# Kernel optimization log

Measured on AMD Instinct MI355X. Metric: run time of the kernel, lower is better.

## Reference

```python
import jax, jax.numpy as jnp
import numpy as np

TOP_K = 2
E = 8      # num_experts
D = 1024   # model dim
F = 2048   # expert hidden dim = int(2*3072/3), already a multiple of 256
B, S = 2, 1024


def setup_inputs() -> dict:
    key = jax.random.key(0)
    ks = jax.random.split(key, 8)
    sc = 0.02
    return {
        "x_bsD": jax.random.normal(ks[0], (B, S, D), dtype=jnp.float32),
        "router_DE": jax.random.normal(ks[1], (D, E), dtype=jnp.float32) * sc,
        "w_in_shared_FD": jax.random.normal(ks[2], (F, D), dtype=jnp.float32) * sc,
        "w_out_shared_DF": jax.random.normal(ks[3], (D, F), dtype=jnp.float32) * sc,
        "w_swiglu_FD": jax.random.normal(ks[4], (F, D), dtype=jnp.float32) * sc,
        "w_in_eDF": jax.random.normal(ks[5], (E, D, F), dtype=jnp.float32) * sc,
        "w_swiglu_eDF": jax.random.normal(ks[6], (E, D, F), dtype=jnp.float32) * sc,
        "w_out_eFD": jax.random.normal(ks[7], (E, F, D), dtype=jnp.float32) * sc,
    }


def reference(x_bsD, router_DE, w_in_shared_FD, w_out_shared_DF, w_swiglu_FD,
              w_in_eDF, w_swiglu_eDF, w_out_eFD):
    b, s, d = x_bsD.shape
    x_aD = x_bsD.reshape(-1, d)                      # [a, D]
    a = x_aD.shape[0]

    # Router (token choice): top-k per token, others masked to -inf
    scores_aE = x_aD @ router_DE                      # [a, E]
    topv_aK, topi_aK = jax.lax.top_k(scores_aE, TOP_K)
    masked_aE = jnp.full_like(scores_aE, -jnp.inf)
    masked_aE = masked_aE.at[jnp.arange(a)[:, None], topi_aK].set(topv_aK)
    # sigmoid(-inf) == 0 -> non-selected (expert, token) pairs contribute nothing
    gates_Ea = jax.nn.sigmoid(masked_aE.astype(jnp.float32)).astype(x_aD.dtype).T  # [E, a]

    # Dispatch: router_indices_EG == arange(a) per expert, so gather == broadcast
    routed_in_EaD = x_aD[None, :, :] * gates_Ea[:, :, None]   # [E, a, D]
    routed_in_EaD = jax.lax.stop_gradient(routed_in_EaD)      # matches .detach()

    # Per-expert bmm SwiGLU
    mid_EaF = jnp.einsum('ead,edf->eaf', routed_in_EaD, w_in_eDF)
    sw_EaF = jnp.einsum('ead,edf->eaf', routed_in_EaD, w_swiglu_eDF)
    h_EaF = jax.nn.silu(mid_EaF) * sw_EaF
    out_EaD = jnp.einsum('eaf,efd->ead', h_EaF, w_out_eFD)

    # Shared expert (computed under torch.no_grad in the original)
    shared_aF = jax.nn.silu(x_aD @ w_in_shared_FD.T) * (x_aD @ w_swiglu_FD.T)
    shared_out_aD = jax.lax.stop_gradient(shared_aF @ w_out_shared_DF.T)

    # Combine: scatter_add with per-expert arange indices == sum over experts
    out_aD = shared_out_aD + jnp.sum(out_EaD, axis=0)
    return out_aD.reshape(b, s, d)
```

## Files before the change

kernel.cpp:

```cpp
#include <hip/hip_runtime.h>
#include <hip/hip_bf16.h>

#define A_TOK 2048
#define DDIM 1024
#define FDIM 2048
#define NEXP 8
#define NE9 9
#define SLOTS_R (2 * A_TOK)
#define SLOTS_T (SLOTS_R + A_TOK)
#define NB1 (2 * FDIM)

#define PREP_TRA_END 8192
#define PREP_TRB_END (PREP_TRA_END + 4096)
#define PREP_SH12_END (PREP_TRB_END + 1024)
#define PREP_SHOUT_END (PREP_SH12_END + 512)
#define PREP_NWG (PREP_SHOUT_END + 512)

typedef __attribute__((ext_vector_type(8))) short short8v;
typedef __attribute__((ext_vector_type(4))) float f32x4;
typedef __attribute__((ext_vector_type(4))) ushort ushort4v;

#define BARRIER() asm volatile("s_barrier" ::: "memory")
#define VMCNT(n) asm volatile("s_waitcnt vmcnt(" #n ")" ::: "memory")

__device__ __forceinline__ void lds16(const void* g, void* l) {
  __builtin_amdgcn_global_load_lds((const __attribute__((address_space(1))) void*)g,
                                   (__attribute__((address_space(3))) void*)l, 16, 0, 0);
}

__device__ __forceinline__ float sigmoidf_(float x) { return 1.f / (1.f + __expf(-x)); }
__device__ __forceinline__ ushort f2bf(float x) {
  __hip_bfloat16 b = __float2bfloat16(x);
  ushort u; __builtin_memcpy(&u, &b, 2); return u;
}
__device__ __forceinline__ float bf2f(ushort u) {
  union { unsigned int i; float f; } x; x.i = (unsigned int)u << 16; return x.f;
}

__global__ void k_prep(const float* __restrict__ w_in_e, const float* __restrict__ w_sw_e,
                       const float* __restrict__ w_out_e, const float* __restrict__ w_in_sh,
                       const float* __restrict__ w_sw_sh, const float* __restrict__ w_out_sh,
                       ushort* __restrict__ wt12, ushort* __restrict__ wt_out_t,
                       const float* __restrict__ x, const float* __restrict__ rw,
                       __hip_bfloat16* __restrict__ xbf, int* __restrict__ top_e,
                       float* __restrict__ top_g) {
  __shared__ ushort tile[64][68];
  int b = blockIdx.x, tid = threadIdx.x;
  if (b < PREP_TRA_END) {
    int z = b >> 9, t2 = b & 511;
    int e = z & 7, which = z >> 3;
    const float* in = (which ? w_sw_e : w_in_e) + (size_t)e * DDIM * FDIM;
    ushort* outb = wt12 + (size_t)e * NB1 * DDIM;
    int c0 = (t2 & 31) * 64, r0 = (t2 >> 5) * 64;
    int rr = tid >> 4, cq = tid & 15;
#pragma unroll
    for (int i = 0; i < 4; i++) {
      int r = i * 16 + rr;
      float4 v = *(const float4*)(in + (size_t)(r0 + r) * FDIM + c0 + cq * 4);
      ushort4v o = {f2bf(v.x), f2bf(v.y), f2bf(v.z), f2bf(v.w)};
      *(ushort4v*)&tile[r][cq * 4] = o;
    }
    __syncthreads();
    int cc = tid >> 4, rq = tid & 15;
#pragma unroll
    for (int i = 0; i < 4; i++) {
      int c = i * 16 + cc;
      int f = c0 + c;
      int rp = ((f >> 5) << 6) + (which << 5) + (f & 31);
      ushort4v o = {tile[rq * 4 + 0][c], tile[rq * 4 + 1][c],
                    tile[rq * 4 + 2][c], tile[rq * 4 + 3][c]};
      *(ushort4v*)(outb + (size_t)rp * DDIM + r0 + rq * 4) = o;
    }
  } else if (b < PREP_TRB_END) {
    int b2 = b - PREP_TRA_END;
    int z = b2 >> 9, t2 = b2 & 511;
    const float* in = w_out_e + (size_t)z * FDIM * DDIM;
    ushort* out = wt_out_t + (size_t)z * DDIM * FDIM;
    int c0 = (t2 & 15) * 64, r0 = (t2 >> 4) * 64;
    int rr = tid >> 4, cq = tid & 15;
#pragma unroll
    for (int i = 0; i < 4; i++) {
      int r = i * 16 + rr;
      float4 v = *(const float4*)(in + (size_t)(r0 + r) * DDIM + c0 + cq * 4);
      ushort4v o = {f2bf(v.x), f2bf(v.y), f2bf(v.z), f2bf(v.w)};
      *(ushort4v*)&tile[r][cq * 4] = o;
    }
    __syncthreads();
    int cc = tid >> 4, rq = tid & 15;
#pragma unroll
    for (int i = 0; i < 4; i++) {
      int c = i * 16 + cc;
      ushort4v o = {tile[rq * 4 + 0][c], tile[rq * 4 + 1][c],
                    tile[rq * 4 + 2][c], tile[rq * 4 + 3][c]};
      *(ushort4v*)(out + (size_t)(c0 + c) * FDIM + r0 + rq * 4) = o;
    }
  } else if (b < PREP_SH12_END) {
    int j = b - PREP_TRB_END;
    int rj = j * 4 + (tid >> 6);
    int l = tid & 63;
    int which = rj & 1, f = rj >> 1;
    const float* src = (which ? w_sw_sh : w_in_sh) + (size_t)f * DDIM;
    int rp = ((f >> 5) << 6) + (which << 5) + (f & 31);
    ushort* dst = wt12 + (size_t)NEXP * NB1 * DDIM + (size_t)rp * DDIM;
#pragma unroll
    for (int i = 0; i < 4; i++) {
      int q = l + 64 * i;
      float4 v = ((const float4*)src)[q];
      ushort4v o = {f2bf(v.x), f2bf(v.y), f2bf(v.z), f2bf(v.w)};
      ((ushort4v*)dst)[q] = o;
    }
  } else if (b < PREP_SHOUT_END) {
    int j = b - PREP_SH12_END;
    int d = j * 2 + (tid >> 7);
    int l = tid & 127;
    const float* src = w_out_sh + (size_t)d * FDIM;
    ushort* dst = wt_out_t + (size_t)NEXP * DDIM * FDIM + (size_t)d * FDIM;
#pragma unroll
    for (int i = 0; i < 4; i++) {
      int q = l + 128 * i;
      float4 v = ((const float4*)src)[q];
      ushort4v o = {f2bf(v.x), f2bf(v.y), f2bf(v.z), f2bf(v.w)};
      ((ushort4v*)dst)[q] = o;
    }
  } else {
    int j = b - PREP_SHOUT_END;
    int t = j * 4 + (tid >> 6);
    int l = tid & 63;
    const float* xr = x + (size_t)t * DDIM;
    float acc[NEXP];
#pragma unroll
    for (int e = 0; e < NEXP; e++) acc[e] = 0.f;
#pragma unroll
    for (int i = 0; i < 16; i++) {
      int d = i * 64 + l;
      float v = xr[d];
      xbf[(size_t)t * DDIM + d] = __float2bfloat16(v);
      const float* rr = rw + (size_t)d * NEXP;
#pragma unroll
      for (int e = 0; e < NEXP; e++) acc[e] += v * rr[e];
    }
#pragma unroll
    for (int e = 0; e < NEXP; e++) {
#pragma unroll
      for (int s = 32; s > 0; s >>= 1) acc[e] += __shfl_xor(acc[e], s);
    }
    if (l == 0) {
      float b1 = -1e30f, b2 = -1e30f;
      int i1 = 0, i2 = 0;
#pragma unroll
      for (int e = 0; e < NEXP; e++) {
        float v = acc[e];
        if (v > b1) { b2 = b1; i2 = i1; b1 = v; i1 = e; }
        else if (v > b2) { b2 = v; i2 = e; }
      }
      top_e[t * 2 + 0] = i1; top_e[t * 2 + 1] = i2;
      top_g[t * 2 + 0] = sigmoidf_(b1); top_g[t * 2 + 1] = sigmoidf_(b2);
    }
  }
}

__global__ void k_scan(const int* __restrict__ top_e, int* __restrict__ counts,
                       int* __restrict__ offs, int* __restrict__ cursor) {
  __shared__ int hist[NEXP];
  int tid = threadIdx.x;
  if (tid < NEXP) hist[tid] = 0;
  __syncthreads();
  for (int i = tid; i < A_TOK * 2; i += 256) atomicAdd(&hist[top_e[i]], 1);
  __syncthreads();
  if (tid == 0) {
    int s = 0;
    for (int e = 0; e < NEXP; e++) { counts[e] = hist[e]; offs[e] = s; s += hist[e]; cursor[e] = 0; }
    counts[NEXP] = A_TOK;
    offs[NEXP] = s;
  }
}

__global__ void k_dispatch(const float* __restrict__ x, const int* __restrict__ top_e,
                           const float* __restrict__ top_g, const int* __restrict__ offs,
                           int* __restrict__ cursor, int* __restrict__ slot_of,
                           __hip_bfloat16* __restrict__ y) {
  int t = blockIdx.x * 4 + (threadIdx.x >> 6);
  int l = threadIdx.x & 63;
  int e0 = top_e[t * 2 + 0], e1 = top_e[t * 2 + 1];
  float g0 = top_g[t * 2 + 0], g1 = top_g[t * 2 + 1];
  int s0 = 0, s1 = 0;
  if (l == 0) {
    s0 = offs[e0] + atomicAdd(&cursor[e0], 1);
    s1 = offs[e1] + atomicAdd(&cursor[e1], 1);
    slot_of[t * 2 + 0] = s0; slot_of[t * 2 + 1] = s1;
  }
  s0 = __shfl(s0, 0); s1 = __shfl(s1, 0);
  const float* xr = x + (size_t)t * DDIM;
#pragma unroll
  for (int i = 0; i < 16; i++) {
    int d = i * 64 + l;
    float v = xr[d];
    y[(size_t)s0 * DDIM + d] = __float2bfloat16(v * g0);
    y[(size_t)s1 * DDIM + d] = __float2bfloat16(v * g1);
  }
}

__global__ __launch_bounds__(256, 3) void k_mlp1(
    const ushort* __restrict__ Abase, const ushort* __restrict__ Bbase,
    ushort* __restrict__ Obase, const int* __restrict__ d_cnt,
    const int* __restrict__ d_off) {
  constexpr int K = DDIM, NT = DDIM / 32;
  constexpr int BUF = 16384;
  __shared__ __align__(16) char smem[3 * BUF];
  int e = blockIdx.z;
  int cnt = d_cnt[e];
  int m0 = blockIdx.y * 128;
  if (m0 >= cnt) return;
  int roff = d_off[e];
  int n0 = blockIdx.x * 128;
  const ushort* B = Bbase + (size_t)e * NB1 * DDIM;
  int tid = threadIdx.x, w = tid >> 6, l = tid & 63;
  int wm = w >> 1, wn = w & 1, lr = l & 15, kg = l >> 4;
  size_t arow0 = (size_t)roff + m0;

  int srow = tid >> 2;
  int sgg = (tid & 3) ^ ((tid >> 3) & 3);
  const ushort* pA0 = Abase + (arow0 + srow) * (size_t)K + sgg * 8;
  const ushort* pA1 = pA0 + (size_t)64 * K;
  const ushort* pB0 = B + ((size_t)n0 + srow) * K + sgg * 8;
  const ushort* pB1 = pB0 + (size_t)64 * K;
  int tls = tid * 16;

  int xorg = (kg ^ ((lr >> 1) & 3)) << 4;
  int offA[4], offB[4];
#pragma unroll
  for (int i = 0; i < 4; i++) {
    offA[i] = (wm * 64 + i * 16 + lr) * 64 + xorg;
    offB[i] = 8192 + (wn * 64 + i * 16 + lr) * 64 + xorg;
  }

  f32x4 acc[4][4];
#pragma unroll
  for (int i = 0; i < 4; i++)
#pragma unroll
    for (int j = 0; j < 4; j++) acc[i][j] = {0.f, 0.f, 0.f, 0.f};

#pragma unroll
  for (int pt = 0; pt < 2; ++pt) {
    char* bb = smem + pt * BUF;
    lds16(pA0, bb + tls);         pA0 += 32;
    lds16(pA1, bb + 4096 + tls);  pA1 += 32;
    lds16(pB0, bb + 8192 + tls);  pB0 += 32;
    lds16(pB1, bb + 12288 + tls); pB1 += 32;
  }
  VMCNT(4);
  BARRIER();

  char* b0 = smem;
  char* b1 = smem + BUF;
  char* b2 = smem + 2 * BUF;
  for (int t = 0; t < NT; ++t) {
    bool st = (t + 2) < NT;
    short8v af[4], bf[4];
#pragma unroll
    for (int mf = 0; mf < 4; mf++) af[mf] = *(const short8v*)(b0 + offA[mf]);
#pragma unroll
    for (int nf = 0; nf < 2; nf++) bf[nf] = *(const short8v*)(b0 + offB[nf]);
    if (st) {
      lds16(pA0, b2 + tls);
      lds16(pA1, b2 + 4096 + tls);
    }
    pA0 += 32; pA1 += 32;
    BARRIER();
    __builtin_amdgcn_s_setprio(1);
#pragma unroll
    for (int nf = 0; nf < 2; nf++)
#pragma unroll
      for (int mf = 0; mf < 4; mf++)
        acc[mf][nf] = __builtin_amdgcn_mfma_f32_16x16x32_bf16(af[mf], bf[nf], acc[mf][nf], 0, 0, 0);
    __builtin_amdgcn_s_setprio(0);
    BARRIER();
#pragma unroll
    for (int nf = 2; nf < 4; nf++) bf[nf] = *(const short8v*)(b0 + offB[nf]);
    if (st) {
      lds16(pB0, b2 + 8192 + tls);
      lds16(pB1, b2 + 12288 + tls);
    }
    pB0 += 32; pB1 += 32;
    BARRIER();
    __builtin_amdgcn_s_setprio(1);
#pragma unroll
    for (int nf = 2; nf < 4; nf++)
#pragma unroll
      for (int mf = 0; mf < 4; mf++)
        acc[mf][nf] = __builtin_amdgcn_mfma_f32_16x16x32_bf16(af[mf], bf[nf], acc[mf][nf], 0, 0, 0);
    __builtin_amdgcn_s_setprio(0);
    if (t < NT - 1) {
      if (st) { VMCNT(4); } else { VMCNT(0); }
      BARRIER();
    }
    char* tmp = b0; b0 = b1; b1 = b2; b2 = tmp;
  }

  int j = (n0 >> 6) + wn;
#pragma unroll
  for (int mf = 0; mf < 4; mf++)
#pragma unroll
    for (int nf = 0; nf < 2; nf++)
#pragma unroll
      for (int r = 0; r < 4; r++) {
        int row = m0 + wm * 64 + mf * 16 + kg * 4 + r;
        if (row < cnt) {
          float mid = acc[mf][nf][r];
          float sw = acc[mf][nf + 2][r];
          float hv = mid * sigmoidf_(mid) * sw;
          int col = j * 32 + nf * 16 + lr;
          Obase[((size_t)roff + row) * FDIM + col] = f2bf(hv);
        }
      }
}

__global__ __launch_bounds__(256, 3) void k_mlp2(
    const ushort* __restrict__ Abase, const ushort* __restrict__ Bbase,
    ushort* __restrict__ part, const int* __restrict__ d_cnt,
    const int* __restrict__ d_off) {
  constexpr int K = FDIM, NT = 1024 / 32;
  constexpr int BUF = 16384;
  __shared__ __align__(16) char smem[3 * BUF];
  int e = blockIdx.z;
  int cnt = d_cnt[e];
  int mt = blockIdx.y >> 1, kz = blockIdx.y & 1;
  int m0 = mt * 128;
  if (m0 >= cnt) return;
  int roff = d_off[e];
  int n0 = blockIdx.x * 128;
  int kbeg = kz * 1024;
  const ushort* B = Bbase + (size_t)e * DDIM * FDIM;
  int tid = threadIdx.x, w = tid >> 6, l = tid & 63;
  int wm = w >> 1, wn = w & 1, lr = l & 15, kg = l >> 4;
  size_t arow0 = (size_t)roff + m0;

  int srow = tid >> 2;
  int sgg = (tid & 3) ^ ((tid >> 3) & 3);
  const ushort* pA0 = Abase + (arow0 + srow) * (size_t)K + kbeg + sgg * 8;
  const ushort* pA1 = pA0 + (size_t)64 * K;
  const ushort* pB0 = B + ((size_t)n0 + srow) * K + kbeg + sgg * 8;
  const ushort* pB1 = pB0 + (size_t)64 * K;
  int tls = tid * 16;

  int xorg = (kg ^ ((lr >> 1) & 3)) << 4;
  int offA[4], offB[4];
#pragma unroll
  for (int i = 0; i < 4; i++) {
    offA[i] = (wm * 64 + i * 16 + lr) * 64 + xorg;
    offB[i] = 8192 + (wn * 64 + i * 16 + lr) * 64 + xorg;
  }

  f32x4 acc[4][4];
#pragma unroll
  for (int i = 0; i < 4; i++)
#pragma unroll
    for (int j = 0; j < 4; j++) acc[i][j] = {0.f, 0.f, 0.f, 0.f};

#pragma unroll
  for (int pt = 0; pt < 2; ++pt) {
    char* bb = smem + pt * BUF;
    lds16(pA0, bb + tls);         pA0 += 32;
    lds16(pA1, bb + 4096 + tls);  pA1 += 32;
    lds16(pB0, bb + 8192 + tls);  pB0 += 32;
    lds16(pB1, bb + 12288 + tls); pB1 += 32;
  }
  VMCNT(4);
  BARRIER();

  char* b0 = smem;
  char* b1 = smem + BUF;
  char* b2 = smem + 2 * BUF;
  for (int t = 0; t < NT; ++t) {
    bool st = (t + 2) < NT;
    short8v af[4], bf[4];
#pragma unroll
    for (int mf = 0; mf < 4; mf++) af[mf] = *(const short8v*)(b0 + offA[mf]);
#pragma unroll
    for (int nf = 0; nf < 2; nf++) bf[nf] = *(const short8v*)(b0 + offB[nf]);
    if (st) {
      lds16(pA0, b2 + tls);
      lds16(pA1, b2 + 4096 + tls);
    }
    pA0 += 32; pA1 += 32;
    BARRIER();
    __builtin_amdgcn_s_setprio(1);
#pragma unroll
    for (int nf = 0; nf < 2; nf++)
#pragma unroll
      for (int mf = 0; mf < 4; mf++)
        acc[mf][nf] = __builtin_amdgcn_mfma_f32_16x16x32_bf16(af[mf], bf[nf], acc[mf][nf], 0, 0, 0);
    __builtin_amdgcn_s_setprio(0);
    BARRIER();
#pragma unroll
    for (int nf = 2; nf < 4; nf++) bf[nf] = *(const short8v*)(b0 + offB[nf]);
    if (st) {
      lds16(pB0, b2 + 8192 + tls);
      lds16(pB1, b2 + 12288 + tls);
    }
    pB0 += 32; pB1 += 32;
    BARRIER();
    __builtin_amdgcn_s_setprio(1);
#pragma unroll
    for (int nf = 2; nf < 4; nf++)
#pragma unroll
      for (int mf = 0; mf < 4; mf++)
        acc[mf][nf] = __builtin_amdgcn_mfma_f32_16x16x32_bf16(af[mf], bf[nf], acc[mf][nf], 0, 0, 0);
    __builtin_amdgcn_s_setprio(0);
    if (t < NT - 1) {
      if (st) { VMCNT(4); } else { VMCNT(0); }
      BARRIER();
    }
    char* tmp = b0; b0 = b1; b1 = b2; b2 = tmp;
  }

  ushort* outp = part + (size_t)kz * SLOTS_T * DDIM;
#pragma unroll
  for (int mf = 0; mf < 4; mf++)
#pragma unroll
    for (int nf = 0; nf < 4; nf++)
#pragma unroll
      for (int r = 0; r < 4; r++) {
        int row = m0 + wm * 64 + mf * 16 + kg * 4 + r;
        if (row < cnt) {
          int col = n0 + wn * 64 + nf * 16 + lr;
          outp[((size_t)roff + row) * DDIM + col] = f2bf(acc[mf][nf][r]);
        }
      }
}

__global__ void k_combine(const ushort* __restrict__ part, const int* __restrict__ slot_of,
                          float* __restrict__ out) {
  int t = blockIdx.x, q = threadIdx.x;
  int rows[3];
  rows[0] = slot_of[t * 2 + 0];
  rows[1] = slot_of[t * 2 + 1];
  rows[2] = SLOTS_R + t;
  size_t P = (size_t)SLOTS_T * DDIM;
  float o[4] = {0.f, 0.f, 0.f, 0.f};
#pragma unroll
  for (int kz = 0; kz < 2; kz++)
#pragma unroll
    for (int i = 0; i < 3; i++) {
      ushort4v v = *(const ushort4v*)(part + kz * P + (size_t)rows[i] * DDIM + q * 4);
#pragma unroll
      for (int j = 0; j < 4; j++) o[j] += bf2f(v[j]);
    }
  float4 ov = {o[0], o[1], o[2], o[3]};
  ((float4*)out)[(size_t)t * (DDIM / 4) + q] = ov;
}

extern "C" void kernel_launch(void* const* d_in, const int* in_sizes, int n_in,
                              void* d_out, int out_size, void* d_ws, size_t ws_size,
                              hipStream_t stream) {
  (void)in_sizes; (void)n_in; (void)out_size; (void)ws_size;
  const float* x        = (const float*)d_in[0];
  const float* router   = (const float*)d_in[1];
  const float* w_in_sh  = (const float*)d_in[2];
  const float* w_out_sh = (const float*)d_in[3];
  const float* w_sw_sh  = (const float*)d_in[4];
  const float* w_in_e   = (const float*)d_in[5];
  const float* w_sw_e   = (const float*)d_in[6];
  const float* w_out_e  = (const float*)d_in[7];
  float* out = (float*)d_out;

  char* ws = (char*)d_ws;
  size_t off = 0;
  auto alloc = [&](size_t bytes) -> char* {
    char* p = ws + off;
    off += (bytes + 255) & ~(size_t)255;
    return p;
  };
  ushort* wt12     = (ushort*)alloc((size_t)NE9 * NB1 * DDIM * 2);
  ushort* wt_out_t = (ushort*)alloc((size_t)NE9 * DDIM * FDIM * 2);
  __hip_bfloat16* y_all = (__hip_bfloat16*)alloc((size_t)SLOTS_R * DDIM * 2);
  __hip_bfloat16* xbf   = (__hip_bfloat16*)alloc((size_t)A_TOK * DDIM * 2);
  ushort* h        = (ushort*)alloc((size_t)SLOTS_T * FDIM * 2);
  int*   counts  = (int*)alloc(64);
  int*   offs    = (int*)alloc(64);
  int*   cursor  = (int*)alloc(64);
  int*   top_e   = (int*)alloc((size_t)A_TOK * 2 * 4);
  float* top_g   = (float*)alloc((size_t)A_TOK * 2 * 4);
  int*   slot_of = (int*)alloc((size_t)A_TOK * 2 * 4);
  (void)alloc(1 << 20);
  ushort* part = wt12;

  k_prep<<<dim3(PREP_NWG), 256, 0, stream>>>(
      w_in_e, w_sw_e, w_out_e, w_in_sh, w_sw_sh, w_out_sh,
      wt12, wt_out_t, x, router, xbf, top_e, top_g);

  k_scan<<<dim3(1), 256, 0, stream>>>(top_e, counts, offs, cursor);

  k_dispatch<<<dim3(A_TOK / 4), 256, 0, stream>>>(x, top_e, top_g, offs, cursor, slot_of, y_all);

  k_mlp1<<<dim3(NB1 / 128, A_TOK / 128, NE9), 256, 0, stream>>>(
      (const ushort*)y_all, wt12, h, counts, offs);

  k_mlp2<<<dim3(DDIM / 128, (A_TOK / 128) * 2, NE9), 256, 0, stream>>>(
      h, wt_out_t, part, counts, offs);

  k_combine<<<dim3(A_TOK), 256, 0, stream>>>(part, slot_of, out);
}
```

Before: 251.2 us.

## Move w_out expert transpose into mlp1 launch and enlarge prep transpose tiles

```diff
diff --git a/kernel.cpp b/kernel.cpp
--- a/kernel.cpp
+++ b/kernel.cpp
@@ -10,9 +10,8 @@
 #define SLOTS_T (SLOTS_R + A_TOK)
 #define NB1 (2 * FDIM)
 
-#define PREP_TRA_END 8192
-#define PREP_TRB_END (PREP_TRA_END + 4096)
-#define PREP_SH12_END (PREP_TRB_END + 1024)
+#define PREP_TRA_END 4096
+#define PREP_SH12_END (PREP_TRA_END + 1024)
 #define PREP_SHOUT_END (PREP_SH12_END + 512)
 #define PREP_NWG (PREP_SHOUT_END + 512)
 
@@ -38,64 +37,44 @@
 }
 
 __global__ void k_prep(const float* __restrict__ w_in_e, const float* __restrict__ w_sw_e,
-                       const float* __restrict__ w_out_e, const float* __restrict__ w_in_sh,
-                       const float* __restrict__ w_sw_sh, const float* __restrict__ w_out_sh,
+                       const float* __restrict__ w_in_sh, const float* __restrict__ w_sw_sh,
+                       const float* __restrict__ w_out_sh,
                        ushort* __restrict__ wt12, ushort* __restrict__ wt_out_t,
                        const float* __restrict__ x, const float* __restrict__ rw,
                        __hip_bfloat16* __restrict__ xbf, int* __restrict__ top_e,
                        float* __restrict__ top_g) {
-  __shared__ ushort tile[64][68];
+  __shared__ ushort tile[128][68];
   int b = blockIdx.x, tid = threadIdx.x;
   if (b < PREP_TRA_END) {
-    int z = b >> 9, t2 = b & 511;
+    int z = b >> 8, p = b & 255;
     int e = z & 7, which = z >> 3;
     const float* in = (which ? w_sw_e : w_in_e) + (size_t)e * DDIM * FDIM;
     ushort* outb = wt12 + (size_t)e * NB1 * DDIM;
-    int c0 = (t2 & 31) * 64, r0 = (t2 >> 5) * 64;
+    int r0 = (p & 7) * 128, c0 = (p >> 3) * 64;
     int rr = tid >> 4, cq = tid & 15;
-#pragma unroll
-    for (int i = 0; i < 4; i++) {
-      int r = i * 16 + rr;
-      float4 v = *(const float4*)(in + (size_t)(r0 + r) * FDIM + c0 + cq * 4);
+    float4 va[8];
+#pragma unroll
+    for (int i = 0; i < 8; i++)
+      va[i] = *(const float4*)(in + (size_t)(r0 + i * 16 + rr) * FDIM + c0 + cq * 4);
+#pragma unroll
+    for (int i = 0; i < 8; i++) {
+      float4 v = va[i];
       ushort4v o = {f2bf(v.x), f2bf(v.y), f2bf(v.z), f2bf(v.w)};
-      *(ushort4v*)&tile[r][cq * 4] = o;
+      *(ushort4v*)&tile[i * 16 + rr][cq * 4] = o;
     }
     __syncthreads();
-    int cc = tid >> 4, rq = tid & 15;
-#pragma unroll
-    for (int i = 0; i < 4; i++) {
-      int c = i * 16 + cc;
+    int cc = tid >> 5, rq = tid & 31;
+#pragma unroll
+    for (int i = 0; i < 8; i++) {
+      int c = i * 8 + cc;
       int f = c0 + c;
       int rp = ((f >> 5) << 6) + (which << 5) + (f & 31);
       ushort4v o = {tile[rq * 4 + 0][c], tile[rq * 4 + 1][c],
                     tile[rq * 4 + 2][c], tile[rq * 4 + 3][c]};
       *(ushort4v*)(outb + (size_t)rp * DDIM + r0 + rq * 4) = o;
     }
-  } else if (b < PREP_TRB_END) {
-    int b2 = b - PREP_TRA_END;
-    int z = b2 >> 9, t2 = b2 & 511;
-    const float* in = w_out_e + (size_t)z * FDIM * DDIM;
-    ushort* out = wt_out_t + (size_t)z * DDIM * FDIM;
-    int c0 = (t2 & 15) * 64, r0 = (t2 >> 4) * 64;
-    int rr = tid >> 4, cq = tid & 15;
-#pragma unroll
-    for (int i = 0; i < 4; i++) {
-      int r = i * 16 + rr;
-      float4 v = *(const float4*)(in + (size_t)(r0 + r) * DDIM + c0 + cq * 4);
-      ushort4v o = {f2bf(v.x), f2bf(v.y), f2bf(v.z), f2bf(v.w)};
-      *(ushort4v*)&tile[r][cq * 4] = o;
-    }
-    __syncthreads();
-    int cc = tid >> 4, rq = tid & 15;
-#pragma unroll
-    for (int i = 0; i < 4; i++) {
-      int c = i * 16 + cc;
-      ushort4v o = {tile[rq * 4 + 0][c], tile[rq * 4 + 1][c],
-                    tile[rq * 4 + 2][c], tile[rq * 4 + 3][c]};
-      *(ushort4v*)(out + (size_t)(c0 + c) * FDIM + r0 + rq * 4) = o;
-    }
   } else if (b < PREP_SH12_END) {
-    int j = b - PREP_TRB_END;
+    int j = b - PREP_TRA_END;
     int rj = j * 4 + (tid >> 6);
     int l = tid & 63;
     int which = rj & 1, f = rj >> 1;
@@ -203,18 +182,50 @@
 __global__ __launch_bounds__(256, 3) void k_mlp1(
     const ushort* __restrict__ Abase, const ushort* __restrict__ Bbase,
     ushort* __restrict__ Obase, const int* __restrict__ d_cnt,
-    const int* __restrict__ d_off) {
+    const int* __restrict__ d_off, const float* __restrict__ w_out_e,
+    ushort* __restrict__ wt_out_t) {
   constexpr int K = DDIM, NT = DDIM / 32;
   constexpr int BUF = 16384;
   __shared__ __align__(16) char smem[3 * BUF];
-  int e = blockIdx.z;
+  int z = blockIdx.z;
+  int tid = threadIdx.x;
+  if (z < 4) {
+    ushort (*tile)[68] = (ushort(*)[68])smem;
+    int jj = (z * 16 + blockIdx.y) * 32 + blockIdx.x;
+    int ex = jj >> 8, p = jj & 255;
+    const float* in = w_out_e + (size_t)ex * FDIM * DDIM;
+    ushort* outp = wt_out_t + (size_t)ex * DDIM * FDIM;
+    int r0 = (p >> 4) * 128, c0 = (p & 15) * 64;
+    int rr = tid >> 4, cq = tid & 15;
+    float4 va[8];
+#pragma unroll
+    for (int i = 0; i < 8; i++)
+      va[i] = *(const float4*)(in + (size_t)(r0 + i * 16 + rr) * DDIM + c0 + cq * 4);
+#pragma unroll
+    for (int i = 0; i < 8; i++) {
+      float4 v = va[i];
+      ushort4v o = {f2bf(v.x), f2bf(v.y), f2bf(v.z), f2bf(v.w)};
+      *(ushort4v*)&tile[i * 16 + rr][cq * 4] = o;
+    }
+    __syncthreads();
+    int cc = tid >> 5, rq = tid & 31;
+#pragma unroll
+    for (int i = 0; i < 8; i++) {
+      int c = i * 8 + cc;
+      ushort4v o = {tile[rq * 4 + 0][c], tile[rq * 4 + 1][c],
+                    tile[rq * 4 + 2][c], tile[rq * 4 + 3][c]};
+      *(ushort4v*)(outp + (size_t)(c0 + c) * FDIM + r0 + rq * 4) = o;
+    }
+    return;
+  }
+  int e = z - 4;
   int cnt = d_cnt[e];
   int m0 = blockIdx.y * 128;
   if (m0 >= cnt) return;
   int roff = d_off[e];
   int n0 = blockIdx.x * 128;
   const ushort* B = Bbase + (size_t)e * NB1 * DDIM;
-  int tid = threadIdx.x, w = tid >> 6, l = tid & 63;
+  int w = tid >> 6, l = tid & 63;
   int wm = w >> 1, wn = w & 1, lr = l & 15, kg = l >> 4;
   size_t arow0 = (size_t)roff + m0;
 
@@ -486,15 +497,15 @@
   ushort* part = wt12;
 
   k_prep<<<dim3(PREP_NWG), 256, 0, stream>>>(
-      w_in_e, w_sw_e, w_out_e, w_in_sh, w_sw_sh, w_out_sh,
+      w_in_e, w_sw_e, w_in_sh, w_sw_sh, w_out_sh,
       wt12, wt_out_t, x, router, xbf, top_e, top_g);
 
   k_scan<<<dim3(1), 256, 0, stream>>>(top_e, counts, offs, cursor);
 
   k_dispatch<<<dim3(A_TOK / 4), 256, 0, stream>>>(x, top_e, top_g, offs, cursor, slot_of, y_all);
 
-  k_mlp1<<<dim3(NB1 / 128, A_TOK / 128, NE9), 256, 0, stream>>>(
-      (const ushort*)y_all, wt12, h, counts, offs);
+  k_mlp1<<<dim3(NB1 / 128, A_TOK / 128, 4 + NE9), 256, 0, stream>>>(
+      (const ushort*)y_all, wt12, h, counts, offs, w_out_e, wt_out_t);
 
   k_mlp2<<<dim3(DDIM / 128, (A_TOK / 128) * 2, NE9), 256, 0, stream>>>(
       h, wt_out_t, part, counts, offs);
```

After: 248.9 us, median of 2. About the same (-0.9%).

## Fuse fp32 weight conversion and transpose into GEMM B-tile loads

Applied to the files above, without the earlier changes.

```diff
diff --git a/kernel.cpp b/kernel.cpp
--- a/kernel.cpp
+++ b/kernel.cpp
@@ -10,18 +10,13 @@
 #define SLOTS_T (SLOTS_R + A_TOK)
 #define NB1 (2 * FDIM)
 
-#define PREP_TRA_END 8192
-#define PREP_TRB_END (PREP_TRA_END + 4096)
-#define PREP_SH12_END (PREP_TRB_END + 1024)
-#define PREP_SHOUT_END (PREP_SH12_END + 512)
-#define PREP_NWG (PREP_SHOUT_END + 512)
-
 typedef __attribute__((ext_vector_type(8))) short short8v;
 typedef __attribute__((ext_vector_type(4))) float f32x4;
 typedef __attribute__((ext_vector_type(4))) ushort ushort4v;
 
 #define BARRIER() asm volatile("s_barrier" ::: "memory")
 #define VMCNT(n) asm volatile("s_waitcnt vmcnt(" #n ")" ::: "memory")
+#define LGKM0() asm volatile("s_waitcnt lgkmcnt(0)" ::: "memory")
 
 __device__ __forceinline__ void lds16(const void* g, void* l) {
   __builtin_amdgcn_global_load_lds((const __attribute__((address_space(1))) void*)g,
@@ -36,126 +31,44 @@
 __device__ __forceinline__ float bf2f(ushort u) {
   union { unsigned int i; float f; } x; x.i = (unsigned int)u << 16; return x.f;
 }
-
-__global__ void k_prep(const float* __restrict__ w_in_e, const float* __restrict__ w_sw_e,
-                       const float* __restrict__ w_out_e, const float* __restrict__ w_in_sh,
-                       const float* __restrict__ w_sw_sh, const float* __restrict__ w_out_sh,
-                       ushort* __restrict__ wt12, ushort* __restrict__ wt_out_t,
-                       const float* __restrict__ x, const float* __restrict__ rw,
-                       __hip_bfloat16* __restrict__ xbf, int* __restrict__ top_e,
-                       float* __restrict__ top_g) {
-  __shared__ ushort tile[64][68];
-  int b = blockIdx.x, tid = threadIdx.x;
-  if (b < PREP_TRA_END) {
-    int z = b >> 9, t2 = b & 511;
-    int e = z & 7, which = z >> 3;
-    const float* in = (which ? w_sw_e : w_in_e) + (size_t)e * DDIM * FDIM;
-    ushort* outb = wt12 + (size_t)e * NB1 * DDIM;
-    int c0 = (t2 & 31) * 64, r0 = (t2 >> 5) * 64;
-    int rr = tid >> 4, cq = tid & 15;
-#pragma unroll
-    for (int i = 0; i < 4; i++) {
-      int r = i * 16 + rr;
-      float4 v = *(const float4*)(in + (size_t)(r0 + r) * FDIM + c0 + cq * 4);
-      ushort4v o = {f2bf(v.x), f2bf(v.y), f2bf(v.z), f2bf(v.w)};
-      *(ushort4v*)&tile[r][cq * 4] = o;
+__device__ __forceinline__ unsigned pk2(float a, float b) {
+  return (unsigned)f2bf(a) | ((unsigned)f2bf(b) << 16);
+}
+
+__global__ void k_router(const float* __restrict__ x, const float* __restrict__ rw,
+                         __hip_bfloat16* __restrict__ xbf, int* __restrict__ top_e,
+                         float* __restrict__ top_g) {
+  int t = blockIdx.x * 4 + (threadIdx.x >> 6);
+  int l = threadIdx.x & 63;
+  const float* xr = x + (size_t)t * DDIM;
+  float acc[NEXP];
+#pragma unroll
+  for (int e = 0; e < NEXP; e++) acc[e] = 0.f;
+#pragma unroll
+  for (int i = 0; i < 16; i++) {
+    int d = i * 64 + l;
+    float v = xr[d];
+    xbf[(size_t)t * DDIM + d] = __float2bfloat16(v);
+    const float* rr = rw + (size_t)d * NEXP;
+#pragma unroll
+    for (int e = 0; e < NEXP; e++) acc[e] += v * rr[e];
+  }
+#pragma unroll
+  for (int e = 0; e < NEXP; e++) {
+#pragma unroll
+    for (int s = 32; s > 0; s >>= 1) acc[e] += __shfl_xor(acc[e], s);
+  }
+  if (l == 0) {
+    float b1 = -1e30f, b2 = -1e30f;
+    int i1 = 0, i2 = 0;
+#pragma unroll
+    for (int e = 0; e < NEXP; e++) {
+      float v = acc[e];
+      if (v > b1) { b2 = b1; i2 = i1; b1 = v; i1 = e; }
+      else if (v > b2) { b2 = v; i2 = e; }
     }
-    __syncthreads();
-    int cc = tid >> 4, rq = tid & 15;
-#pragma unroll
-    for (int i = 0; i < 4; i++) {
-      int c = i * 16 + cc;
-      int f = c0 + c;
-      int rp = ((f >> 5) << 6) + (which << 5) + (f & 31);
-      ushort4v o = {tile[rq * 4 + 0][c], tile[rq * 4 + 1][c],
-                    tile[rq * 4 + 2][c], tile[rq * 4 + 3][c]};
-      *(ushort4v*)(outb + (size_t)rp * DDIM + r0 + rq * 4) = o;
-    }
-  } else if (b < PREP_TRB_END) {
-    int b2 = b - PREP_TRA_END;
-    int z = b2 >> 9, t2 = b2 & 511;
-    const float* in = w_out_e + (size_t)z * FDIM * DDIM;
-    ushort* out = wt_out_t + (size_t)z * DDIM * FDIM;
-    int c0 = (t2 & 15) * 64, r0 = (t2 >> 4) * 64;
-    int rr = tid >> 4, cq = tid & 15;
-#pragma unroll
-    for (int i = 0; i < 4; i++) {
-      int r = i * 16 + rr;
-      float4 v = *(const float4*)(in + (size_t)(r0 + r) * DDIM + c0 + cq * 4);
-      ushort4v o = {f2bf(v.x), f2bf(v.y), f2bf(v.z), f2bf(v.w)};
-      *(ushort4v*)&tile[r][cq * 4] = o;
-    }
-    __syncthreads();
-    int cc = tid >> 4, rq = tid & 15;
-#pragma unroll
-    for (int i = 0; i < 4; i++) {
-      int c = i * 16 + cc;
-      ushort4v o = {tile[rq * 4 + 0][c], tile[rq * 4 + 1][c],
-                    tile[rq * 4 + 2][c], tile[rq * 4 + 3][c]};
-      *(ushort4v*)(out + (size_t)(c0 + c) * FDIM + r0 + rq * 4) = o;
-    }
-  } else if (b < PREP_SH12_END) {
-    int j = b - PREP_TRB_END;
-    int rj = j * 4 + (tid >> 6);
-    int l = tid & 63;
-    int which = rj & 1, f = rj >> 1;
-    const float* src = (which ? w_sw_sh : w_in_sh) + (size_t)f * DDIM;
-    int rp = ((f >> 5) << 6) + (which << 5) + (f & 31);
-    ushort* dst = wt12 + (size_t)NEXP * NB1 * DDIM + (size_t)rp * DDIM;
-#pragma unroll
-    for (int i = 0; i < 4; i++) {
-      int q = l + 64 * i;
-      float4 v = ((const float4*)src)[q];
-      ushort4v o = {f2bf(v.x), f2bf(v.y), f2bf(v.z), f2bf(v.w)};
-      ((ushort4v*)dst)[q] = o;
-    }
-  } else if (b < PREP_SHOUT_END) {
-    int j = b - PREP_SH12_END;
-    int d = j * 2 + (tid >> 7);
-    int l = tid & 127;
-    const float* src = w_out_sh + (size_t)d * FDIM;
-    ushort* dst = wt_out_t + (size_t)NEXP * DDIM * FDIM + (size_t)d * FDIM;
-#pragma unroll
-    for (int i = 0; i < 4; i++) {
-      int q = l + 128 * i;
-      float4 v = ((const float4*)src)[q];
-      ushort4v o = {f2bf(v.x), f2bf(v.y), f2bf(v.z), f2bf(v.w)};
-      ((ushort4v*)dst)[q] = o;
-    }
-  } else {
-    int j = b - PREP_SHOUT_END;
-    int t = j * 4 + (tid >> 6);
-    int l = tid & 63;
-    const float* xr = x + (size_t)t * DDIM;
-    float acc[NEXP];
-#pragma unroll
-    for (int e = 0; e < NEXP; e++) acc[e] = 0.f;
-#pragma unroll
-    for (int i = 0; i < 16; i++) {
-      int d = i * 64 + l;
-      float v = xr[d];
-      xbf[(size_t)t * DDIM + d] = __float2bfloat16(v);
-      const float* rr = rw + (size_t)d * NEXP;
-#pragma unroll
-      for (int e = 0; e < NEXP; e++) acc[e] += v * rr[e];
-    }
-#pragma unroll
-    for (int e = 0; e < NEXP; e++) {
-#pragma unroll
-      for (int s = 32; s > 0; s >>= 1) acc[e] += __shfl_xor(acc[e], s);
-    }
-    if (l == 0) {
-      float b1 = -1e30f, b2 = -1e30f;
-      int i1 = 0, i2 = 0;
-#pragma unroll
-      for (int e = 0; e < NEXP; e++) {
-        float v = acc[e];
-        if (v > b1) { b2 = b1; i2 = i1; b1 = v; i1 = e; }
-        else if (v > b2) { b2 = v; i2 = e; }
-      }
-      top_e[t * 2 + 0] = i1; top_e[t * 2 + 1] = i2;
-      top_g[t * 2 + 0] = sigmoidf_(b1); top_g[t * 2 + 1] = sigmoidf_(b2);
-    }
+    top_e[t * 2 + 0] = i1; top_e[t * 2 + 1] = i2;
+    top_g[t * 2 + 0] = sigmoidf_(b1); top_g[t * 2 + 1] = sigmoidf_(b2);
   }
 }
 
@@ -200,10 +113,36 @@
   }
 }
 
+#define LOADB(r0, r1, r2, r3) { \
+    r0 = *(const f32x4*)(pB); \
+    r1 = *(const f32x4*)(pB + bst); \
+    r2 = *(const f32x4*)(pB + 2 * bst); \
+    r3 = *(const f32x4*)(pB + 3 * bst); \
+    pB += badv; }
+
+#define WRITEB(dst, r0, r1, r2, r3) { \
+    uint2 q0, q1, q2, q3; \
+    if (!shared_e) {  \
+      q0 = {pk2(r0[0], r1[0]), pk2(r2[0], r3[0])}; \
+      q1 = {pk2(r0[1], r1[1]), pk2(r2[1], r3[1])}; \
+      q2 = {pk2(r0[2], r1[2]), pk2(r2[2], r3[2])}; \
+      q3 = {pk2(r0[3], r1[3]), pk2(r2[3], r3[3])}; \
+    } else {      \
+      q0 = {pk2(r0[0], r0[1]), pk2(r0[2], r0[3])}; \
+      q1 = {pk2(r1[0], r1[1]), pk2(r1[2], r1[3])}; \
+      q2 = {pk2(r2[0], r2[1]), pk2(r2[2], r2[3])}; \
+      q3 = {pk2(r3[0], r3[1]), pk2(r3[2], r3[3])}; \
+    } \
+    *(uint2*)((dst) + wofs[0]) = q0; \
+    *(uint2*)((dst) + wofs[1]) = q1; \
+    *(uint2*)((dst) + wofs[2]) = q2; \
+    *(uint2*)((dst) + wofs[3]) = q3; }
+
 __global__ __launch_bounds__(256, 3) void k_mlp1(
-    const ushort* __restrict__ Abase, const ushort* __restrict__ Bbase,
-    ushort* __restrict__ Obase, const int* __restrict__ d_cnt,
-    const int* __restrict__ d_off) {
+    const ushort* __restrict__ Abase, const float* __restrict__ w_in_e,
+    const float* __restrict__ w_sw_e, const float* __restrict__ w_in_sh,
+    const float* __restrict__ w_sw_sh, ushort* __restrict__ Obase,
+    const int* __restrict__ d_cnt, const int* __restrict__ d_off) {
   constexpr int K = DDIM, NT = DDIM / 32;
   constexpr int BUF = 16384;
   __shared__ __align__(16) char smem[3 * BUF];
@@ -213,7 +152,6 @@
   if (m0 >= cnt) return;
   int roff = d_off[e];
   int n0 = blockIdx.x * 128;
-  const ushort* B = Bbase + (size_t)e * NB1 * DDIM;
   int tid = threadIdx.x, w = tid >> 6, l = tid & 63;
   int wm = w >> 1, wn = w & 1, lr = l & 15, kg = l >> 4;
   size_t arow0 = (size_t)roff + m0;
@@ -222,9 +160,30 @@
   int sgg = (tid & 3) ^ ((tid >> 3) & 3);
   const ushort* pA0 = Abase + (arow0 + srow) * (size_t)K + sgg * 8;
   const ushort* pA1 = pA0 + (size_t)64 * K;
-  const ushort* pB0 = B + ((size_t)n0 + srow) * K + sgg * 8;
-  const ushort* pB1 = pB0 + (size_t)64 * K;
   int tls = tid * 16;
+
+  int kq = tid & 7, nq = tid >> 3;
+  int nl0 = nq * 4;
+  int nprime = n0 + nl0;
+  int which = (nprime >> 5) & 1;
+  int f0 = ((nprime >> 6) << 5) + (nprime & 31);
+  bool shared_e = (e == NEXP);
+  const float* pB;
+  size_t bst; int badv;
+  if (!shared_e) {
+    pB = (which ? w_sw_e : w_in_e) + (size_t)e * DDIM * FDIM + (size_t)(kq * 4) * FDIM + f0;
+    bst = FDIM; badv = 32 * FDIM;
+  } else {
+    pB = (which ? w_sw_sh : w_in_sh) + (size_t)f0 * DDIM + kq * 4;
+    bst = DDIM; badv = 32;
+  }
+  int wofs[4];
+#pragma unroll
+  for (int j = 0; j < 4; j++) {
+    int row = nl0 + j;
+    int s = (((kq >> 1) ^ ((row >> 1) & 3)) << 1) | (kq & 1);
+    wofs[j] = 8192 + row * 64 + s * 8;
+  }
 
   int xorg = (kg ^ ((lr >> 1) & 3)) << 4;
   int offA[4], offB[4];
@@ -240,61 +199,95 @@
 #pragma unroll
     for (int j = 0; j < 4; j++) acc[i][j] = {0.f, 0.f, 0.f, 0.f};
 
-#pragma unroll
-  for (int pt = 0; pt < 2; ++pt) {
-    char* bb = smem + pt * BUF;
-    lds16(pA0, bb + tls);         pA0 += 32;
-    lds16(pA1, bb + 4096 + tls);  pA1 += 32;
-    lds16(pB0, bb + 8192 + tls);  pB0 += 32;
-    lds16(pB1, bb + 12288 + tls); pB1 += 32;
-  }
-  VMCNT(4);
+  f32x4 sA0, sA1, sA2, sA3, sB0, sB1, sB2, sB3;
+
+  char* p0 = smem;
+  char* p1 = smem + BUF;
+  char* p2 = smem + 2 * BUF;
+
+  lds16(pA0, p0 + tls); lds16(pA1, p0 + 4096 + tls); pA0 += 32; pA1 += 32;
+  LOADB(sA0, sA1, sA2, sA3);
+  lds16(pA0, p1 + tls); lds16(pA1, p1 + 4096 + tls); pA0 += 32; pA1 += 32;
+  LOADB(sB0, sB1, sB2, sB3);
+  VMCNT(6);
+  WRITEB(p0, sA0, sA1, sA2, sA3);
+  LGKM0();
   BARRIER();
 
-  char* b0 = smem;
-  char* b1 = smem + BUF;
-  char* b2 = smem + 2 * BUF;
-  for (int t = 0; t < NT; ++t) {
-    bool st = (t + 2) < NT;
-    short8v af[4], bf[4];
-#pragma unroll
-    for (int mf = 0; mf < 4; mf++) af[mf] = *(const short8v*)(b0 + offA[mf]);
-#pragma unroll
-    for (int nf = 0; nf < 2; nf++) bf[nf] = *(const short8v*)(b0 + offB[nf]);
-    if (st) {
-      lds16(pA0, b2 + tls);
-      lds16(pA1, b2 + 4096 + tls);
+  for (int t = 0; t < NT; t += 2) {
+    {
+      bool st = (t + 2) < NT;
+      short8v af[4], bf[4];
+#pragma unroll
+      for (int i = 0; i < 4; i++) af[i] = *(const short8v*)(p0 + offA[i]);
+#pragma unroll
+      for (int i = 0; i < 2; i++) bf[i] = *(const short8v*)(p0 + offB[i]);
+      if (st) { lds16(pA0, p2 + tls); lds16(pA1, p2 + 4096 + tls); }
+      pA0 += 32; pA1 += 32;
+      BARRIER();
+      __builtin_amdgcn_s_setprio(1);
+#pragma unroll
+      for (int nf = 0; nf < 2; nf++)
+#pragma unroll
+        for (int mf = 0; mf < 4; mf++)
+          acc[mf][nf] = __builtin_amdgcn_mfma_f32_16x16x32_bf16(af[mf], bf[nf], acc[mf][nf], 0, 0, 0);
+      __builtin_amdgcn_s_setprio(0);
+      BARRIER();
+#pragma unroll
+      for (int i = 2; i < 4; i++) bf[i] = *(const short8v*)(p0 + offB[i]);
+      if (st) { LOADB(sA0, sA1, sA2, sA3); }
+      BARRIER();
+      __builtin_amdgcn_s_setprio(1);
+#pragma unroll
+      for (int nf = 2; nf < 4; nf++)
+#pragma unroll
+        for (int mf = 0; mf < 4; mf++)
+          acc[mf][nf] = __builtin_amdgcn_mfma_f32_16x16x32_bf16(af[mf], bf[nf], acc[mf][nf], 0, 0, 0);
+      __builtin_amdgcn_s_setprio(0);
+      if (st) { VMCNT(6); } else { VMCNT(0); }
+      WRITEB(p1, sB0, sB1, sB2, sB3);
+      LGKM0();
+      BARRIER();
+      char* tp = p0; p0 = p1; p1 = p2; p2 = tp;
     }
-    pA0 += 32; pA1 += 32;
-    BARRIER();
-    __builtin_amdgcn_s_setprio(1);
-#pragma unroll
-    for (int nf = 0; nf < 2; nf++)
-#pragma unroll
-      for (int mf = 0; mf < 4; mf++)
-        acc[mf][nf] = __builtin_amdgcn_mfma_f32_16x16x32_bf16(af[mf], bf[nf], acc[mf][nf], 0, 0, 0);
-    __builtin_amdgcn_s_setprio(0);
-    BARRIER();
-#pragma unroll
-    for (int nf = 2; nf < 4; nf++) bf[nf] = *(const short8v*)(b0 + offB[nf]);
-    if (st) {
-      lds16(pB0, b2 + 8192 + tls);
-      lds16(pB1, b2 + 12288 + tls);
+    {
+      bool st = (t + 3) < NT;
+      bool last = (t + 1) == NT - 1;
+      short8v af[4], bf[4];
+#pragma unroll
+      for (int i = 0; i < 4; i++) af[i] = *(const short8v*)(p0 + offA[i]);
+#pragma unroll
+      for (int i = 0; i < 2; i++) bf[i] = *(const short8v*)(p0 + offB[i]);
+      if (st) { lds16(pA0, p2 + tls); lds16(pA1, p2 + 4096 + tls); }
+      pA0 += 32; pA1 += 32;
+      BARRIER();
+      __builtin_amdgcn_s_setprio(1);
+#pragma unroll
+      for (int nf = 0; nf < 2; nf++)
+#pragma unroll
+        for (int mf = 0; mf < 4; mf++)
+          acc[mf][nf] = __builtin_amdgcn_mfma_f32_16x16x32_bf16(af[mf], bf[nf], acc[mf][nf], 0, 0, 0);
+      __builtin_amdgcn_s_setprio(0);
+      BARRIER();
+#pragma unroll
+      for (int i = 2; i < 4; i++) bf[i] = *(const short8v*)(p0 + offB[i]);
+      if (st) { LOADB(sB0, sB1, sB2, sB3); }
+      BARRIER();
+      __builtin_amdgcn_s_setprio(1);
+#pragma unroll
+      for (int nf = 2; nf < 4; nf++)
+#pragma unroll
+        for (int mf = 0; mf < 4; mf++)
+          acc[mf][nf] = __builtin_amdgcn_mfma_f32_16x16x32_bf16(af[mf], bf[nf], acc[mf][nf], 0, 0, 0);
+      __builtin_amdgcn_s_setprio(0);
+      if (!last) {
+        if (st) { VMCNT(6); } else { VMCNT(0); }
+        WRITEB(p1, sA0, sA1, sA2, sA3);
+        LGKM0();
+        BARRIER();
+        char* tp = p0; p0 = p1; p1 = p2; p2 = tp;
+      }
     }
-    pB0 += 32; pB1 += 32;
-    BARRIER();
-    __builtin_amdgcn_s_setprio(1);
-#pragma unroll
-    for (int nf = 2; nf < 4; nf++)
-#pragma unroll
-      for (int mf = 0; mf < 4; mf++)
-        acc[mf][nf] = __builtin_amdgcn_mfma_f32_16x16x32_bf16(af[mf], bf[nf], acc[mf][nf], 0, 0, 0);
-    __builtin_amdgcn_s_setprio(0);
-    if (t < NT - 1) {
-      if (st) { VMCNT(4); } else { VMCNT(0); }
-      BARRIER();
-    }
-    char* tmp = b0; b0 = b1; b1 = b2; b2 = tmp;
   }
 
   int j = (n0 >> 6) + wn;
@@ -316,9 +309,9 @@
 }
 
 __global__ __launch_bounds__(256, 3) void k_mlp2(
-    const ushort* __restrict__ Abase, const ushort* __restrict__ Bbase,
-    ushort* __restrict__ part, const int* __restrict__ d_cnt,
-    const int* __restrict__ d_off) {
+    const ushort* __restrict__ Abase, const float* __restrict__ w_out_e,
+    const float* __restrict__ w_out_sh, ushort* __restrict__ part,
+    const int* __restrict__ d_cnt, const int* __restrict__ d_off) {
   constexpr int K = FDIM, NT = 1024 / 32;
   constexpr int BUF = 16384;
   __shared__ __align__(16) char smem[3 * BUF];
@@ -330,7 +323,6 @@
   int roff = d_off[e];
   int n0 = blockIdx.x * 128;
   int kbeg = kz * 1024;
-  const ushort* B = Bbase + (size_t)e * DDIM * FDIM;
   int tid = threadIdx.x, w = tid >> 6, l = tid & 63;
   int wm = w >> 1, wn = w & 1, lr = l & 15, kg = l >> 4;
   size_t arow0 = (size_t)roff + m0;
@@ -339,9 +331,28 @@
   int sgg = (tid & 3) ^ ((tid >> 3) & 3);
   const ushort* pA0 = Abase + (arow0 + srow) * (size_t)K + kbeg + sgg * 8;
   const ushort* pA1 = pA0 + (size_t)64 * K;
-  const ushort* pB0 = B + ((size_t)n0 + srow) * K + kbeg + sgg * 8;
-  const ushort* pB1 = pB0 + (size_t)64 * K;
   int tls = tid * 16;
+
+  int kq = tid & 7, nq = tid >> 3;
+  int nl0 = nq * 4;
+  int nprime = n0 + nl0;
+  bool shared_e = (e == NEXP);
+  const float* pB;
+  size_t bst; int badv;
+  if (!shared_e) {
+    pB = w_out_e + (size_t)e * FDIM * DDIM + (size_t)(kbeg + kq * 4) * DDIM + nprime;
+    bst = DDIM; badv = 32 * DDIM;
+  } else {
+    pB = w_out_sh + (size_t)nprime * FDIM + kbeg + kq * 4;
+    bst = FDIM; badv = 32;
+  }
+  int wofs[4];
+#pragma unroll
+  for (int j = 0; j < 4; j++) {
+    int row = nl0 + j;
+    int s = (((kq >> 1) ^ ((row >> 1) & 3)) << 1) | (kq & 1);
+    wofs[j] = 8192 + row * 64 + s * 8;
+  }
 
   int xorg = (kg ^ ((lr >> 1) & 3)) << 4;
   int offA[4], offB[4];
@@ -357,61 +368,95 @@
 #pragma unroll
     for (int j = 0; j < 4; j++) acc[i][j] = {0.f, 0.f, 0.f, 0.f};
 
-#pragma unroll
-  for (int pt = 0; pt < 2; ++pt) {
-    char* bb = smem + pt * BUF;
-    lds16(pA0, bb + tls);         pA0 += 32;
-    lds16(pA1, bb + 4096 + tls);  pA1 += 32;
-    lds16(pB0, bb + 8192 + tls);  pB0 += 32;
-    lds16(pB1, bb + 12288 + tls); pB1 += 32;
-  }
-  VMCNT(4);
+  f32x4 sA0, sA1, sA2, sA3, sB0, sB1, sB2, sB3;
+
+  char* p0 = smem;
+  char* p1 = smem + BUF;
+  char* p2 = smem + 2 * BUF;
+
+  lds16(pA0, p0 + tls); lds16(pA1, p0 + 4096 + tls); pA0 += 32; pA1 += 32;
+  LOADB(sA0, sA1, sA2, sA3);
+  lds16(pA0, p1 + tls); lds16(pA1, p1 + 4096 + tls); pA0 += 32; pA1 += 32;
+  LOADB(sB0, sB1, sB2, sB3);
+  VMCNT(6);
+  WRITEB(p0, sA0, sA1, sA2, sA3);
+  LGKM0();
   BARRIER();
 
-  char* b0 = smem;
-  char* b1 = smem + BUF;
-  char* b2 = smem + 2 * BUF;
-  for (int t = 0; t < NT; ++t) {
-    bool st = (t + 2) < NT;
-    short8v af[4], bf[4];
-#pragma unroll
-    for (int mf = 0; mf < 4; mf++) af[mf] = *(const short8v*)(b0 + offA[mf]);
-#pragma unroll
-    for (int nf = 0; nf < 2; nf++) bf[nf] = *(const short8v*)(b0 + offB[nf]);
-    if (st) {
-      lds16(pA0, b2 + tls);
-      lds16(pA1, b2 + 4096 + tls);
+  for (int t = 0; t < NT; t += 2) {
+    {
+      bool st = (t + 2) < NT;
+      short8v af[4], bf[4];
+#pragma unroll
+      for (int i = 0; i < 4; i++) af[i] = *(const short8v*)(p0 + offA[i]);
+#pragma unroll
+      for (int i = 0; i < 2; i++) bf[i] = *(const short8v*)(p0 + offB[i]);
+      if (st) { lds16(pA0, p2 + tls); lds16(pA1, p2 + 4096 + tls); }
+      pA0 += 32; pA1 += 32;
+      BARRIER();
+      __builtin_amdgcn_s_setprio(1);
+#pragma unroll
+      for (int nf = 0; nf < 2; nf++)
+#pragma unroll
+        for (int mf = 0; mf < 4; mf++)
+          acc[mf][nf] = __builtin_amdgcn_mfma_f32_16x16x32_bf16(af[mf], bf[nf], acc[mf][nf], 0, 0, 0);
+      __builtin_amdgcn_s_setprio(0);
+      BARRIER();
+#pragma unroll
+      for (int i = 2; i < 4; i++) bf[i] = *(const short8v*)(p0 + offB[i]);
+      if (st) { LOADB(sA0, sA1, sA2, sA3); }
+      BARRIER();
+      __builtin_amdgcn_s_setprio(1);
+#pragma unroll
+      for (int nf = 2; nf < 4; nf++)
+#pragma unroll
+        for (int mf = 0; mf < 4; mf++)
+          acc[mf][nf] = __builtin_amdgcn_mfma_f32_16x16x32_bf16(af[mf], bf[nf], acc[mf][nf], 0, 0, 0);
+      __builtin_amdgcn_s_setprio(0);
+      if (st) { VMCNT(6); } else { VMCNT(0); }
+      WRITEB(p1, sB0, sB1, sB2, sB3);
+      LGKM0();
+      BARRIER();
+      char* tp = p0; p0 = p1; p1 = p2; p2 = tp;
     }
-    pA0 += 32; pA1 += 32;
-    BARRIER();
-    __builtin_amdgcn_s_setprio(1);
-#pragma unroll
-    for (int nf = 0; nf < 2; nf++)
-#pragma unroll
-      for (int mf = 0; mf < 4; mf++)
-        acc[mf][nf] = __builtin_amdgcn_mfma_f32_16x16x32_bf16(af[mf], bf[nf], acc[mf][nf], 0, 0, 0);
-    __builtin_amdgcn_s_setprio(0);
-    BARRIER();
-#pragma unroll
-    for (int nf = 2; nf < 4; nf++) bf[nf] = *(const short8v*)(b0 + offB[nf]);
-    if (st) {
-      lds16(pB0, b2 + 8192 + tls);
-      lds16(pB1, b2 + 12288 + tls);
+    {
+      bool st = (t + 3) < NT;
+      bool last = (t + 1) == NT - 1;
+      short8v af[4], bf[4];
+#pragma unroll
+      for (int i = 0; i < 4; i++) af[i] = *(const short8v*)(p0 + offA[i]);
+#pragma unroll
+      for (int i = 0; i < 2; i++) bf[i] = *(const short8v*)(p0 + offB[i]);
+      if (st) { lds16(pA0, p2 + tls); lds16(pA1, p2 + 4096 + tls); }
+      pA0 += 32; pA1 += 32;
+      BARRIER();
+      __builtin_amdgcn_s_setprio(1);
+#pragma unroll
+      for (int nf = 0; nf < 2; nf++)
+#pragma unroll
+        for (int mf = 0; mf < 4; mf++)
+          acc[mf][nf] = __builtin_amdgcn_mfma_f32_16x16x32_bf16(af[mf], bf[nf], acc[mf][nf], 0, 0, 0);
+      __builtin_amdgcn_s_setprio(0);
+      BARRIER();
+#pragma unroll
+      for (int i = 2; i < 4; i++) bf[i] = *(const short8v*)(p0 + offB[i]);
+      if (st) { LOADB(sB0, sB1, sB2, sB3); }
+      BARRIER();
+      __builtin_amdgcn_s_setprio(1);
+#pragma unroll
+      for (int nf = 2; nf < 4; nf++)
+#pragma unroll
+        for (int mf = 0; mf < 4; mf++)
+          acc[mf][nf] = __builtin_amdgcn_mfma_f32_16x16x32_bf16(af[mf], bf[nf], acc[mf][nf], 0, 0, 0);
+      __builtin_amdgcn_s_setprio(0);
+      if (!last) {
+        if (st) { VMCNT(6); } else { VMCNT(0); }
+        WRITEB(p1, sA0, sA1, sA2, sA3);
+        LGKM0();
+        BARRIER();
+        char* tp = p0; p0 = p1; p1 = p2; p2 = tp;
+      }
     }
-    pB0 += 32; pB1 += 32;
-    BARRIER();
-    __builtin_amdgcn_s_setprio(1);
-#pragma unroll
-    for (int nf = 2; nf < 4; nf++)
-#pragma unroll
-      for (int mf = 0; mf < 4; mf++)
-        acc[mf][nf] = __builtin_amdgcn_mfma_f32_16x16x32_bf16(af[mf], bf[nf], acc[mf][nf], 0, 0, 0);
-    __builtin_amdgcn_s_setprio(0);
-    if (t < NT - 1) {
-      if (st) { VMCNT(4); } else { VMCNT(0); }
-      BARRIER();
-    }
-    char* tmp = b0; b0 = b1; b1 = b2; b2 = tmp;
   }
 
   ushort* outp = part + (size_t)kz * SLOTS_T * DDIM;
@@ -471,11 +516,10 @@
     off += (bytes + 255) & ~(size_t)255;
     return p;
   };
-  ushort* wt12     = (ushort*)alloc((size_t)NE9 * NB1 * DDIM * 2);
-  ushort* wt_out_t = (ushort*)alloc((size_t)NE9 * DDIM * FDIM * 2);
   __hip_bfloat16* y_all = (__hip_bfloat16*)alloc((size_t)SLOTS_R * DDIM * 2);
   __hip_bfloat16* xbf   = (__hip_bfloat16*)alloc((size_t)A_TOK * DDIM * 2);
-  ushort* h        = (ushort*)alloc((size_t)SLOTS_T * FDIM * 2);
+  ushort* h    = (ushort*)alloc((size_t)SLOTS_T * FDIM * 2);
+  ushort* part = (ushort*)alloc((size_t)2 * SLOTS_T * DDIM * 2);
   int*   counts  = (int*)alloc(64);
   int*   offs    = (int*)alloc(64);
   int*   cursor  = (int*)alloc(64);
@@ -483,21 +527,13 @@
   float* top_g   = (float*)alloc((size_t)A_TOK * 2 * 4);
   int*   slot_of = (int*)alloc((size_t)A_TOK * 2 * 4);
   (void)alloc(1 << 20);
-  ushort* part = wt12;
-
-  k_prep<<<dim3(PREP_NWG), 256, 0, stream>>>(
-      w_in_e, w_sw_e, w_out_e, w_in_sh, w_sw_sh, w_out_sh,
-      wt12, wt_out_t, x, router, xbf, top_e, top_g);
-
+
+  k_router<<<dim3(A_TOK / 4), 256, 0, stream>>>(x, router, xbf, top_e, top_g);
   k_scan<<<dim3(1), 256, 0, stream>>>(top_e, counts, offs, cursor);
-
   k_dispatch<<<dim3(A_TOK / 4), 256, 0, stream>>>(x, top_e, top_g, offs, cursor, slot_of, y_all);
-
   k_mlp1<<<dim3(NB1 / 128, A_TOK / 128, NE9), 256, 0, stream>>>(
-      (const ushort*)y_all, wt12, h, counts, offs);
-
+      (const ushort*)y_all, w_in_e, w_sw_e, w_in_sh, w_sw_sh, h, counts, offs);
   k_mlp2<<<dim3(DDIM / 128, (A_TOK / 128) * 2, NE9), 256, 0, stream>>>(
-      h, wt_out_t, part, counts, offs);
-
+      h, w_out_e, w_out_sh, part, counts, offs);
   k_combine<<<dim3(A_TOK), 256, 0, stream>>>(part, slot_of, out);
 }
```

Result: slower. 285.7 us (+13.7%).
